# Kernel tuning notes

Hardware: AMD Instinct MI355X
Metric: run time of the kernel (lower is better)

Reference implementation:

```python
import jax, jax.numpy as jnp
import numpy as np

LOG_2PI = float(np.log(2.0 * np.pi))


def _logmatexp(logA, v):
    # log( A @ exp(v) ) per batch row: [K,K] x [B,K] -> [B,K]
    return jax.nn.logsumexp(logA[None, :, :] + v[:, None, :], axis=-1)


def setup_inputs() -> dict:
    key = jax.random.key(0)
    k1, k2, k3, k4, k5 = jax.random.split(key, 5)
    B, T, K = 32, 8192, 64
    obvs = jax.random.normal(k1, (B, T), dtype=jnp.float32)
    log_initial_probs = jax.random.normal(k2, (K,), dtype=jnp.float32)
    # transfer = exp(randn) in the torch module -> strictly positive matrix
    transfer = jnp.exp(jax.random.normal(k3, (K, K), dtype=jnp.float32))
    means = jax.random.normal(k4, (K,), dtype=jnp.float32)
    log_stds = 0.1 * jax.random.normal(k5, (K,), dtype=jnp.float32)
    return {
        "obvs": obvs,
        "log_initial_probs": log_initial_probs,
        "transfer": transfer,
        "means": means,
        "log_stds": log_stds,
    }


def reference(obvs, log_initial_probs, transfer, means, log_stds):
    B, T = obvs.shape
    K = log_initial_probs.shape[0]

    # GaussianEmbedding: per-state scalar Gaussian log-density -> [B, T, K]
    x = obvs[..., None]  # [B, T, 1]
    inv_std = jnp.exp(-log_stds)
    z = (x - means) * inv_std
    ln_e = -0.5 * z * z - log_stds - 0.5 * LOG_2PI  # [B, T, K]

    logA = jnp.log(transfer)  # [K, K]
    ln_e_t = jnp.swapaxes(ln_e, 0, 1)  # [T, B, K] for scan

    # ---- forward recurrence ----
    f0 = ln_e_t[0] + log_initial_probs  # [B, K]

    def fwd_step(f_prev, e_i):
        f_i = e_i + _logmatexp(logA, f_prev)
        return f_i, f_i

    _, f_rest = jax.lax.scan(fwd_step, f0, ln_e_t[1:])
    ln_fs = jnp.concatenate([f0[None], f_rest], axis=0)  # [T, B, K]

    # ---- backward recurrence ----
    bT = jnp.broadcast_to(log_initial_probs, (B, K))

    def bwd_step(b_next, e_next):
        b_i = _logmatexp(logA, b_next + e_next)
        return b_i, b_i

    # steps ii = T-2 .. 0 use ln_e[ii+1]; scan over ln_e_t[1:] reversed
    _, b_rev = jax.lax.scan(bwd_step, bT, ln_e_t[1:], reverse=True)
    ln_bs = jnp.concatenate([b_rev, bT[None]], axis=0)  # [T, B, K]

    log_gamma = ln_fs + ln_bs  # [T, B, K]
    log_gamma = log_gamma - jax.nn.logsumexp(log_gamma, axis=-1, keepdims=True)
    return jnp.swapaxes(log_gamma, 0, 1)  # [B, T, K]
```

## Files before the change

kernel.cpp:

```cpp
#include <hip/hip_runtime.h>
#include <math.h>

#define HMM_B 32
#define HMM_T 8192
#define HMM_K 64
#define L_EFF 512
#define L_WARM 384
#define C_CHUNKS (HMM_T / L_EFF)

typedef float f2v __attribute__((ext_vector_type(2)));

#define LN2F 0.69314718055994531f
#define INV_LN2F 1.4426950408889634f
#define HALF_INV_LN2_SQRTF 0.8493218002880191f
#define NEG_HALF_LOG_2PI 0.91893853320467274f

__device__ __forceinline__ float bcast0(float v) {
    return __int_as_float(__builtin_amdgcn_readfirstlane(__float_as_int(v)));
}
__device__ __forceinline__ float exp2_fast(float x) {
    float r; asm("v_exp_f32 %0, %1" : "=v"(r) : "v"(x)); return r;
}
__device__ __forceinline__ float log2_fast(float x) {
    float r; asm("v_log_f32 %0, %1" : "=v"(r) : "v"(x)); return r;
}

__device__ __forceinline__ float matvec_row(const f2v* __restrict__ areg,
                                            const float4* __restrict__ wv) {
    f2v a0 = {0.f,0.f}, a1 = {0.f,0.f}, a2 = {0.f,0.f}, a3 = {0.f,0.f};
    #pragma unroll
    for (int j = 0; j < 8; ++j) {
        float4 wA = wv[2 * j];
        float4 wB = wv[2 * j + 1];
        f2v t;
        t.x = wA.x; t.y = wA.y; a0 += areg[4 * j + 0] * t;
        t.x = wA.z; t.y = wA.w; a1 += areg[4 * j + 1] * t;
        t.x = wB.x; t.y = wB.y; a2 += areg[4 * j + 2] * t;
        t.x = wB.z; t.y = wB.w; a3 += areg[4 * j + 3] * t;
    }
    f2v s = (a0 + a1) + (a2 + a3);
    return s.x + s.y;
}

#define FWD_STEP { \
    float d_ = fminf(v - bcast0(v), 100.0f); \
    float w_ = exp2_fast(d_); \
    *wbs = w_; \
    __builtin_amdgcn_wave_barrier(); \
    float xn_ = ow[t + 1]; \
    float zn_ = (xn_ - mean_k) * inv_std2; \
    float e2n_ = fmaf(-zn_, zn_, ce2); \
    float u_ = matvec_row(areg, wbuf4); \
    __builtin_amdgcn_wave_barrier(); \
    v = e2c + log2_fast(u_); \
    e2c = e2n_; }

#define BWD_STEP { \
    float tmp_ = v + e2c; \
    float d_ = fminf(tmp_ - bcast0(tmp_), 100.0f); \
    float w_ = exp2_fast(d_); \
    *wbs = w_; \
    __builtin_amdgcn_wave_barrier(); \
    float xn_ = ow[t - 1]; \
    float zn_ = (xn_ - mean_k) * inv_std2; \
    float e2n_ = fmaf(-zn_, zn_, ce2); \
    float u_ = matvec_row(areg, wbuf4); \
    __builtin_amdgcn_wave_barrier(); \
    v = log2_fast(u_); \
    e2c = e2n_; }

__global__ void __launch_bounds__(64, 1)
hmm_recur_chunk(const float* __restrict__ obvs,
                const float* __restrict__ log_init,
                const float* __restrict__ transfer,
                const float* __restrict__ means,
                const float* __restrict__ log_stds,
                float* __restrict__ f_out,
                float* __restrict__ b_out)
{
    __shared__ float4 wbuf4[16];
    __shared__ float obs_lds[1024];
    const int lane = threadIdx.x;
    int blk = blockIdx.x;
    const bool is_fwd = blk < HMM_B * C_CHUNKS;
    if (!is_fwd) blk -= HMM_B * C_CHUNKS;
    const int b  = blk >> 4;
    const int c  = blk & (C_CHUNKS - 1);
    const int t0 = c * L_EFF;
    const int tE = t0 + L_EFF;

    const float mean_k   = means[lane];
    const float ls       = log_stds[lane];
    const float inv_std2 = __expf(-ls) * HALF_INV_LN2_SQRTF;
    const float ce2      = (-ls - NEG_HALF_LOG_2PI) * INV_LN2F;
    const float li2      = log_init[lane] * INV_LN2F;

    f2v areg[32];
    const f2v* Arow = (const f2v*)(transfer + lane * HMM_K);
    #pragma unroll
    for (int j = 0; j < 32; ++j) areg[j] = Arow[j];

    const float* __restrict__ orow = obvs + (size_t)b * HMM_T;
    const int w_lo = is_fwd ? ((c == 0) ? 0 : ((t0 - L_WARM) & ~3)) : t0;
    int nfl = HMM_T - w_lo; if (nfl > 1024) nfl = 1024;
    {
        const float4* o4 = (const float4*)(orow + w_lo);
        float4* l4 = (float4*)obs_lds;
        for (int i = lane; i < (nfl >> 2); i += 64) l4[i] = o4[i];
    }
    __syncthreads();
    const float* ow = obs_lds - w_lo;
    float* wbs = ((float*)wbuf4) + lane;

    if (is_fwd) {
        const int t_s = (c == 0) ? 0 : (t0 - L_WARM);
        float x0 = ow[t_s];
        float z0 = (x0 - mean_k) * inv_std2;
        float v  = fmaf(-z0, z0, ce2) + ((c == 0) ? li2 : 0.0f);
        float* po;
        if (c == 0) {
            po = f_out + ((size_t)b * HMM_T + 0) * HMM_K + lane;
            *po = v;
        } else {
            po = f_out + ((size_t)b * HMM_T + (t0 - 1)) * HMM_K + lane;
        }
        float x1 = ow[t_s + 1];
        float z1 = (x1 - mean_k) * inv_std2;
        float e2c = fmaf(-z1, z1, ce2);
        int t = t_s + 1;
        for (; t < t0; ++t) {
            FWD_STEP
        }
        for (; t < tE; ++t) {
            FWD_STEP
            po += HMM_K; *po = v;
        }
    } else {
        const bool last = (c == C_CHUNKS - 1);
        int t = last ? (HMM_T - 1) : (tE - 1 + L_WARM);
        float v;
        float* po;
        if (last) {
            v = li2;
            po = b_out + ((size_t)b * HMM_T + (HMM_T - 1)) * HMM_K + lane;
            *po = v;
        } else {
            v = 0.0f;
            po = b_out + ((size_t)b * HMM_T + tE) * HMM_K + lane;
        }
        float xs = ow[t];
        float zs = (xs - mean_k) * inv_std2;
        float e2c = fmaf(-zs, zs, ce2);
        for (; t > tE; --t) {
            BWD_STEP
        }
        for (; t > t0; --t) {
            BWD_STEP
            po -= HMM_K; *po = v;
        }
    }
}

__global__ void __launch_bounds__(256)
hmm_combine(const float* __restrict__ fbuf,
            const float* __restrict__ bbuf,
            float* __restrict__ out)
{
    const size_t row = (size_t)blockIdx.x * 4 + (threadIdx.x >> 6);
    const int lane = threadIdx.x & 63;
    const size_t idx = row * HMM_K + lane;
    float g = fbuf[idx] + bbuf[idx];
    float m = g;
    #pragma unroll
    for (int off = 32; off > 0; off >>= 1) m = fmaxf(m, __shfl_xor(m, off));
    float e = exp2_fast(g - m);
    float s = e;
    #pragma unroll
    for (int off = 32; off > 0; off >>= 1) s += __shfl_xor(s, off);
    out[idx] = LN2F * ((g - m) - log2_fast(s));
}

__global__ void __launch_bounds__(64, 1)
hmm_fwd_single(const float* __restrict__ obvs,
               const float* __restrict__ log_init,
               const float* __restrict__ transfer,
               const float* __restrict__ means,
               const float* __restrict__ log_stds,
               float* __restrict__ f_out)
{
    __shared__ float4 wbuf4[16];
    __shared__ float obs_lds_full[HMM_T + 4];
    const int lane = threadIdx.x;
    const int b = blockIdx.x;
    const float mean_k   = means[lane];
    const float ls       = log_stds[lane];
    const float inv_std2 = __expf(-ls) * HALF_INV_LN2_SQRTF;
    const float ce2      = (-ls - NEG_HALF_LOG_2PI) * INV_LN2F;
    const float li2      = log_init[lane] * INV_LN2F;
    f2v areg[32];
    const f2v* Arow = (const f2v*)(transfer + lane * HMM_K);
    #pragma unroll
    for (int j = 0; j < 32; ++j) areg[j] = Arow[j];
    const float* __restrict__ orow = obvs + (size_t)b * HMM_T;
    {
        const float4* o4 = (const float4*)orow;
        float4* l4 = (float4*)obs_lds_full;
        #pragma unroll 4
        for (int i = lane; i < HMM_T / 4; i += 64) l4[i] = o4[i];
    }
    __syncthreads();
    const float* ow = obs_lds_full;
    float* wbs = ((float*)wbuf4) + lane;
    float x0 = ow[0];
    float z0 = (x0 - mean_k) * inv_std2;
    float v  = fmaf(-z0, z0, ce2) + li2;
    float* po = f_out + (size_t)b * HMM_T * HMM_K + lane;
    *po = v;
    float x1 = ow[1];
    float z1 = (x1 - mean_k) * inv_std2;
    float e2c = fmaf(-z1, z1, ce2);
    for (int t = 1; t < HMM_T; ++t) {
        FWD_STEP
        po += HMM_K; *po = v;
    }
}

__global__ void __launch_bounds__(64, 1)
hmm_bwd_combine(const float* __restrict__ obvs,
                const float* __restrict__ log_init,
                const float* __restrict__ transfer,
                const float* __restrict__ means,
                const float* __restrict__ log_stds,
                float* __restrict__ fout)
{
    __shared__ float4 wbuf4[16];
    __shared__ float obs_lds_full[HMM_T + 4];
    const int lane = threadIdx.x;
    const int b = blockIdx.x;
    const float mean_k   = means[lane];
    const float ls       = log_stds[lane];
    const float inv_std2 = __expf(-ls) * HALF_INV_LN2_SQRTF;
    const float ce2      = (-ls - NEG_HALF_LOG_2PI) * INV_LN2F;
    const float li2      = log_init[lane] * INV_LN2F;
    f2v areg[32];
    const f2v* Arow = (const f2v*)(transfer + lane * HMM_K);
    #pragma unroll
    for (int j = 0; j < 32; ++j) areg[j] = Arow[j];
    const float* __restrict__ orow = obvs + (size_t)b * HMM_T;
    {
        const float4* o4 = (const float4*)orow;
        float4* l4 = (float4*)obs_lds_full;
        #pragma unroll 4
        for (int i = lane; i < HMM_T / 4; i += 64) l4[i] = o4[i];
    }
    __syncthreads();
    const float* ow = obs_lds_full;
    float* wbs = ((float*)wbuf4) + lane;
    float bb = li2;
    for (int t = HMM_T - 1; t >= 0; --t) {
        const size_t base = ((size_t)b * HMM_T + t) * HMM_K;
        float g = fout[base + lane] + bb;
        float m = g;
        #pragma unroll
        for (int off = 32; off > 0; off >>= 1) m = fmaxf(m, __shfl_xor(m, off));
        float e = exp2_fast(g - m);
        float s = e;
        #pragma unroll
        for (int off = 32; off > 0; off >>= 1) s += __shfl_xor(s, off);
        fout[base + lane] = LN2F * ((g - m) - log2_fast(s));
        if (t > 0) {
            float xt = ow[t];
            float zt = (xt - mean_k) * inv_std2;
            float tmp = bb + fmaf(-zt, zt, ce2);
            float d = fminf(tmp - bcast0(tmp), 100.0f);
            float w = exp2_fast(d);
            *wbs = w;
            __builtin_amdgcn_wave_barrier();
            float u = matvec_row(areg, wbuf4);
            __builtin_amdgcn_wave_barrier();
            bb = log2_fast(u);
        }
    }
}

extern "C" void kernel_launch(void* const* d_in, const int* in_sizes, int n_in,
                              void* d_out, int out_size, void* d_ws, size_t ws_size,
                              hipStream_t stream)
{
    const float* obvs     = (const float*)d_in[0];
    const float* log_init = (const float*)d_in[1];
    const float* transfer = (const float*)d_in[2];
    const float* means    = (const float*)d_in[3];
    const float* log_stds = (const float*)d_in[4];
    float* out = (float*)d_out;

    const size_t need = (size_t)HMM_B * HMM_T * HMM_K * sizeof(float);
    if (ws_size >= need) {
        float* bws = (float*)d_ws;
        hipLaunchKernelGGL(hmm_recur_chunk, dim3(2 * HMM_B * C_CHUNKS), dim3(HMM_K), 0, stream,
                           obvs, log_init, transfer, means, log_stds, out, bws);
        hipLaunchKernelGGL(hmm_combine, dim3(HMM_B * HMM_T / 4), dim3(256), 0, stream,
                           out, bws, out);
    } else {
        hipLaunchKernelGGL(hmm_fwd_single, dim3(HMM_B), dim3(HMM_K), 0, stream,
                           obvs, log_init, transfer, means, log_stds, out);
        hipLaunchKernelGGL(hmm_bwd_combine, dim3(HMM_B), dim3(HMM_K), 0, stream,
                           obvs, log_init, transfer, means, log_stds, out);
    }
}
```

Baseline: 315.6 us.

## Replace broadcast LDS reads in matvec with per-quad loads plus DPP rotation

The per-step 64x64 matvec previously had every lane read all 16 float4 entries of the shared weight buffer. Now each lane reads only 4 float4s, picked by its position within a quad, and the other values are rotated across the quad with DPP row rotates. The transfer-matrix registers are permuted at load time to match. The goal is fewer LDS reads on the serial recurrence critical path, at the cost of 12 DPP moves per matvec and extra dependency latency.

```diff
diff --git a/kernel.cpp b/kernel.cpp
--- a/kernel.cpp
+++ b/kernel.cpp
@@ -8,8 +8,6 @@
 #define L_WARM 384
 #define C_CHUNKS (HMM_T / L_EFF)
 
-typedef float f2v __attribute__((ext_vector_type(2)));
-
 #define LN2F 0.69314718055994531f
 #define INV_LN2F 1.4426950408889634f
 #define HALF_INV_LN2_SQRTF 0.8493218002880191f
@@ -24,22 +22,48 @@
 __device__ __forceinline__ float log2_fast(float x) {
     float r; asm("v_log_f32 %0, %1" : "=v"(r) : "v"(x)); return r;
 }
-
-__device__ __forceinline__ float matvec_row(const f2v* __restrict__ areg,
-                                            const float4* __restrict__ wv) {
-    f2v a0 = {0.f,0.f}, a1 = {0.f,0.f}, a2 = {0.f,0.f}, a3 = {0.f,0.f};
+__device__ __forceinline__ float dpp_rot4(float v) {
+    return __int_as_float(__builtin_amdgcn_update_dpp(0, __float_as_int(v), 0x39, 0xF, 0xF, true));
+}
+
+__device__ __forceinline__ float matvec_quad(const float4 (&areg4)[4][4],
+                                             const float4* __restrict__ wbuf4,
+                                             int q) {
+    float4 ch0 = wbuf4[q];
+    float4 ch1 = wbuf4[q + 4];
+    float4 ch2 = wbuf4[q + 8];
+    float4 ch3 = wbuf4[q + 12];
+    float a0 = 0.f, a1 = 0.f, a2 = 0.f, a3 = 0.f;
+    float4 ch[4] = {ch0, ch1, ch2, ch3};
     #pragma unroll
-    for (int j = 0; j < 8; ++j) {
-        float4 wA = wv[2 * j];
-        float4 wB = wv[2 * j + 1];
-        f2v t;
-        t.x = wA.x; t.y = wA.y; a0 += areg[4 * j + 0] * t;
-        t.x = wA.z; t.y = wA.w; a1 += areg[4 * j + 1] * t;
-        t.x = wB.x; t.y = wB.y; a2 += areg[4 * j + 2] * t;
-        t.x = wB.z; t.y = wB.w; a3 += areg[4 * j + 3] * t;
-    }
-    f2v s = (a0 + a1) + (a2 + a3);
-    return s.x + s.y;
+    for (int r = 0; r < 4; ++r) {
+        float4 c = ch[r];
+        #pragma unroll
+        for (int s = 0; s < 4; ++s) {
+            if (s) {
+                c.x = dpp_rot4(c.x);
+                c.y = dpp_rot4(c.y);
+                c.z = dpp_rot4(c.z);
+                c.w = dpp_rot4(c.w);
+            }
+            a0 = fmaf(areg4[r][s].x, c.x, a0);
+            a1 = fmaf(areg4[r][s].y, c.y, a1);
+            a2 = fmaf(areg4[r][s].z, c.z, a2);
+            a3 = fmaf(areg4[r][s].w, c.w, a3);
+        }
+    }
+    return (a0 + a1) + (a2 + a3);
+}
+
+__device__ __forceinline__ void load_areg(const float* __restrict__ transfer, int lane,
+                                          float4 (&areg4)[4][4]) {
+    const float4* Arow4 = (const float4*)(transfer + (size_t)lane * HMM_K);
+    const int q = lane & 3;
+    #pragma unroll
+    for (int r = 0; r < 4; ++r)
+        #pragma unroll
+        for (int s = 0; s < 4; ++s)
+            areg4[r][s] = Arow4[(((q + s) & 3)) + 4 * r];
 }
 
 #define FWD_STEP { \
@@ -47,11 +71,11 @@
     float w_ = exp2_fast(d_); \
     *wbs = w_; \
     __builtin_amdgcn_wave_barrier(); \
+    float u_ = matvec_quad(areg4, wbuf4, q); \
+    __builtin_amdgcn_wave_barrier(); \
     float xn_ = ow[t + 1]; \
     float zn_ = (xn_ - mean_k) * inv_std2; \
     float e2n_ = fmaf(-zn_, zn_, ce2); \
-    float u_ = matvec_row(areg, wbuf4); \
-    __builtin_amdgcn_wave_barrier(); \
     v = e2c + log2_fast(u_); \
     e2c = e2n_; }
 
@@ -61,11 +85,11 @@
     float w_ = exp2_fast(d_); \
     *wbs = w_; \
     __builtin_amdgcn_wave_barrier(); \
+    float u_ = matvec_quad(areg4, wbuf4, q); \
+    __builtin_amdgcn_wave_barrier(); \
     float xn_ = ow[t - 1]; \
     float zn_ = (xn_ - mean_k) * inv_std2; \
     float e2n_ = fmaf(-zn_, zn_, ce2); \
-    float u_ = matvec_row(areg, wbuf4); \
-    __builtin_amdgcn_wave_barrier(); \
     v = log2_fast(u_); \
     e2c = e2n_; }
 
@@ -81,6 +105,7 @@
     __shared__ float4 wbuf4[16];
     __shared__ float obs_lds[1024];
     const int lane = threadIdx.x;
+    const int q = lane & 3;
     int blk = blockIdx.x;
     const bool is_fwd = blk < HMM_B * C_CHUNKS;
     if (!is_fwd) blk -= HMM_B * C_CHUNKS;
@@ -95,10 +120,8 @@
     const float ce2      = (-ls - NEG_HALF_LOG_2PI) * INV_LN2F;
     const float li2      = log_init[lane] * INV_LN2F;
 
-    f2v areg[32];
-    const f2v* Arow = (const f2v*)(transfer + lane * HMM_K);
-    #pragma unroll
-    for (int j = 0; j < 32; ++j) areg[j] = Arow[j];
+    float4 areg4[4][4];
+    load_areg(transfer, lane, areg4);
 
     const float* __restrict__ orow = obvs + (size_t)b * HMM_T;
     const int w_lo = is_fwd ? ((c == 0) ? 0 : ((t0 - L_WARM) & ~3)) : t0;
@@ -191,16 +214,15 @@
     __shared__ float4 wbuf4[16];
     __shared__ float obs_lds_full[HMM_T + 4];
     const int lane = threadIdx.x;
+    const int q = lane & 3;
     const int b = blockIdx.x;
     const float mean_k   = means[lane];
     const float ls       = log_stds[lane];
     const float inv_std2 = __expf(-ls) * HALF_INV_LN2_SQRTF;
     const float ce2      = (-ls - NEG_HALF_LOG_2PI) * INV_LN2F;
     const float li2      = log_init[lane] * INV_LN2F;
-    f2v areg[32];
-    const f2v* Arow = (const f2v*)(transfer + lane * HMM_K);
-    #pragma unroll
-    for (int j = 0; j < 32; ++j) areg[j] = Arow[j];
+    float4 areg4[4][4];
+    load_areg(transfer, lane, areg4);
     const float* __restrict__ orow = obvs + (size_t)b * HMM_T;
     {
         const float4* o4 = (const float4*)orow;
@@ -236,16 +258,15 @@
     __shared__ float4 wbuf4[16];
     __shared__ float obs_lds_full[HMM_T + 4];
     const int lane = threadIdx.x;
+    const int q = lane & 3;
     const int b = blockIdx.x;
     const float mean_k   = means[lane];
     const float ls       = log_stds[lane];
     const float inv_std2 = __expf(-ls) * HALF_INV_LN2_SQRTF;
     const float ce2      = (-ls - NEG_HALF_LOG_2PI) * INV_LN2F;
     const float li2      = log_init[lane] * INV_LN2F;
-    f2v areg[32];
-    const f2v* Arow = (const f2v*)(transfer + lane * HMM_K);
-    #pragma unroll
-    for (int j = 0; j < 32; ++j) areg[j] = Arow[j];
+    float4 areg4[4][4];
+    load_areg(transfer, lane, areg4);
     const float* __restrict__ orow = obvs + (size_t)b * HMM_T;
     {
         const float4* o4 = (const float4*)orow;
@@ -276,7 +297,7 @@
             float w = exp2_fast(d);
             *wbs = w;
             __builtin_amdgcn_wave_barrier();
-            float u = matvec_row(areg, wbuf4);
+            float u = matvec_quad(areg4, wbuf4, q);
             __builtin_amdgcn_wave_barrier();
             bb = log2_fast(u);
         }
```

Result: slower. 423.3 us (+34.1%).

## Halve LDS broadcast reads in matvec using v_permlane32_swap exchange

Applied to the files above, without the earlier changes.

Each half-wave now reads only its 32-element half of the shared weight vector from LDS, and the two halves swap values across lanes with v_permlane32_swap. The packed f2v FMAs become scalar FMAs against a 64-entry per-lane transfer row. A runtime probe detects the swap semantics and XOR-permutes how the row is loaded. The aim is to cut LDS read traffic and latency on the serial recurrence critical path, at the cost of extra permlane instructions, more scalar FMAs, and a dependence on exact permlane behaviour.

```diff
diff --git a/kernel.cpp b/kernel.cpp
--- a/kernel.cpp
+++ b/kernel.cpp
@@ -7,8 +7,7 @@
 #define L_EFF 512
 #define L_WARM 384
 #define C_CHUNKS (HMM_T / L_EFF)
-
-typedef float f2v __attribute__((ext_vector_type(2)));
+#define OBS_WIN 1024
 
 #define LN2F 0.69314718055994531f
 #define INV_LN2F 1.4426950408889634f
@@ -24,22 +23,49 @@
 __device__ __forceinline__ float log2_fast(float x) {
     float r; asm("v_log_f32 %0, %1" : "=v"(r) : "v"(x)); return r;
 }
-
-__device__ __forceinline__ float matvec_row(const f2v* __restrict__ areg,
-                                            const float4* __restrict__ wv) {
-    f2v a0 = {0.f,0.f}, a1 = {0.f,0.f}, a2 = {0.f,0.f}, a3 = {0.f,0.f};
-    #pragma unroll
-    for (int j = 0; j < 8; ++j) {
-        float4 wA = wv[2 * j];
-        float4 wB = wv[2 * j + 1];
-        f2v t;
-        t.x = wA.x; t.y = wA.y; a0 += areg[4 * j + 0] * t;
-        t.x = wA.z; t.y = wA.w; a1 += areg[4 * j + 1] * t;
-        t.x = wB.x; t.y = wB.y; a2 += areg[4 * j + 2] * t;
-        t.x = wB.z; t.y = wB.w; a3 += areg[4 * j + 3] * t;
-    }
-    f2v s = (a0 + a1) + (a2 + a3);
-    return s.x + s.y;
+__device__ __forceinline__ void pl32_swap(float& a, float& b) {
+    asm("v_permlane32_swap_b32 %0, %1" : "+v"(a), "+v"(b));
+}
+
+__device__ __forceinline__ int probe_flip(int hs) {
+    float pa = (float)(1 + hs);
+    float pb = pa;
+    pl32_swap(pa, pb);
+    return (bcast0(pa) == 2.0f) ? 0 : 1;
+}
+
+__device__ __forceinline__ float matvec_swap(const float* __restrict__ areg,
+                                             const float4* __restrict__ wbuf4,
+                                             int hs ) {
+    float4 c[8];
+    const float4* base = wbuf4 + (hs << 3);
+    #pragma unroll
+    for (int k = 0; k < 8; ++k) c[k] = base[k];
+    float a0 = 0.f, a1 = 0.f, a2 = 0.f, a3 = 0.f;
+    #pragma unroll
+    for (int k = 0; k < 8; ++k) {
+        float xh = c[k].x, xl = c[k].x; pl32_swap(xh, xl);
+        float yh = c[k].y, yl = c[k].y; pl32_swap(yh, yl);
+        float zh = c[k].z, zl = c[k].z; pl32_swap(zh, zl);
+        float wh = c[k].w, wl = c[k].w; pl32_swap(wh, wl);
+        a0 = fmaf(areg[4 * k + 0], xl, a0);
+        a1 = fmaf(areg[4 * k + 1], yl, a1);
+        a2 = fmaf(areg[4 * k + 2], zl, a2);
+        a3 = fmaf(areg[4 * k + 3], wl, a3);
+        a0 = fmaf(areg[32 + 4 * k + 0], xh, a0);
+        a1 = fmaf(areg[32 + 4 * k + 1], yh, a1);
+        a2 = fmaf(areg[32 + 4 * k + 2], zh, a2);
+        a3 = fmaf(areg[32 + 4 * k + 3], wh, a3);
+    }
+    return (a0 + a1) + (a2 + a3);
+}
+
+__device__ __forceinline__ void load_areg(const float* __restrict__ transfer,
+                                          int lane, int flip, float* areg) {
+    const int xorm = flip ? 32 : 0;
+    #pragma unroll
+    for (int j = 0; j < HMM_K; ++j)
+        areg[j] = transfer[lane * HMM_K + (j ^ xorm)];
 }
 
 #define FWD_STEP { \
@@ -47,11 +73,11 @@
     float w_ = exp2_fast(d_); \
     *wbs = w_; \
     __builtin_amdgcn_wave_barrier(); \
+    float u_ = matvec_swap(areg, wbuf4, hs); \
+    __builtin_amdgcn_wave_barrier(); \
     float xn_ = ow[t + 1]; \
     float zn_ = (xn_ - mean_k) * inv_std2; \
     float e2n_ = fmaf(-zn_, zn_, ce2); \
-    float u_ = matvec_row(areg, wbuf4); \
-    __builtin_amdgcn_wave_barrier(); \
     v = e2c + log2_fast(u_); \
     e2c = e2n_; }
 
@@ -61,11 +87,11 @@
     float w_ = exp2_fast(d_); \
     *wbs = w_; \
     __builtin_amdgcn_wave_barrier(); \
+    float u_ = matvec_swap(areg, wbuf4, hs); \
+    __builtin_amdgcn_wave_barrier(); \
     float xn_ = ow[t - 1]; \
     float zn_ = (xn_ - mean_k) * inv_std2; \
     float e2n_ = fmaf(-zn_, zn_, ce2); \
-    float u_ = matvec_row(areg, wbuf4); \
-    __builtin_amdgcn_wave_barrier(); \
     v = log2_fast(u_); \
     e2c = e2n_; }
 
@@ -79,8 +105,9 @@
                 float* __restrict__ b_out)
 {
     __shared__ float4 wbuf4[16];
-    __shared__ float obs_lds[1024];
+    __shared__ float obs_lds[OBS_WIN];
     const int lane = threadIdx.x;
+    const int hs = lane >> 5;
     int blk = blockIdx.x;
     const bool is_fwd = blk < HMM_B * C_CHUNKS;
     if (!is_fwd) blk -= HMM_B * C_CHUNKS;
@@ -95,14 +122,13 @@
     const float ce2      = (-ls - NEG_HALF_LOG_2PI) * INV_LN2F;
     const float li2      = log_init[lane] * INV_LN2F;
 
-    f2v areg[32];
-    const f2v* Arow = (const f2v*)(transfer + lane * HMM_K);
-    #pragma unroll
-    for (int j = 0; j < 32; ++j) areg[j] = Arow[j];
+    const int flip = probe_flip(hs);
+    float areg[HMM_K];
+    load_areg(transfer, lane, flip, areg);
 
     const float* __restrict__ orow = obvs + (size_t)b * HMM_T;
     const int w_lo = is_fwd ? ((c == 0) ? 0 : ((t0 - L_WARM) & ~3)) : t0;
-    int nfl = HMM_T - w_lo; if (nfl > 1024) nfl = 1024;
+    int nfl = HMM_T - w_lo; if (nfl > OBS_WIN) nfl = OBS_WIN;
     {
         const float4* o4 = (const float4*)(orow + w_lo);
         float4* l4 = (float4*)obs_lds;
@@ -191,16 +217,16 @@
     __shared__ float4 wbuf4[16];
     __shared__ float obs_lds_full[HMM_T + 4];
     const int lane = threadIdx.x;
+    const int hs = lane >> 5;
     const int b = blockIdx.x;
     const float mean_k   = means[lane];
     const float ls       = log_stds[lane];
     const float inv_std2 = __expf(-ls) * HALF_INV_LN2_SQRTF;
     const float ce2      = (-ls - NEG_HALF_LOG_2PI) * INV_LN2F;
     const float li2      = log_init[lane] * INV_LN2F;
-    f2v areg[32];
-    const f2v* Arow = (const f2v*)(transfer + lane * HMM_K);
-    #pragma unroll
-    for (int j = 0; j < 32; ++j) areg[j] = Arow[j];
+    const int flip = probe_flip(hs);
+    float areg[HMM_K];
+    load_areg(transfer, lane, flip, areg);
     const float* __restrict__ orow = obvs + (size_t)b * HMM_T;
     {
         const float4* o4 = (const float4*)orow;
@@ -236,16 +262,16 @@
     __shared__ float4 wbuf4[16];
     __shared__ float obs_lds_full[HMM_T + 4];
     const int lane = threadIdx.x;
+    const int hs = lane >> 5;
     const int b = blockIdx.x;
     const float mean_k   = means[lane];
     const float ls       = log_stds[lane];
     const float inv_std2 = __expf(-ls) * HALF_INV_LN2_SQRTF;
     const float ce2      = (-ls - NEG_HALF_LOG_2PI) * INV_LN2F;
     const float li2      = log_init[lane] * INV_LN2F;
-    f2v areg[32];
-    const f2v* Arow = (const f2v*)(transfer + lane * HMM_K);
-    #pragma unroll
-    for (int j = 0; j < 32; ++j) areg[j] = Arow[j];
+    const int flip = probe_flip(hs);
+    float areg[HMM_K];
+    load_areg(transfer, lane, flip, areg);
     const float* __restrict__ orow = obvs + (size_t)b * HMM_T;
     {
         const float4* o4 = (const float4*)orow;
@@ -276,7 +302,7 @@
             float w = exp2_fast(d);
             *wbs = w;
             __builtin_amdgcn_wave_barrier();
-            float u = matvec_row(areg, wbuf4);
+            float u = matvec_swap(areg, wbuf4, hs);
             __builtin_amdgcn_wave_barrier();
             bb = log2_fast(u);
         }
```

Measured after the change: 608.5 us. +92.8%, slower.
